# Optimization experiments

Measured on AMD Instinct MI355X. Metric: run time of the kernel, lower is better.

The kernel has to match this reference:

```python
import jax, jax.numpy as jnp
import numpy as np

B, T, D = 2, 2048, 1024
HD = 128          # head_dim
NH = 16           # num_attention_heads
NKV = 8           # num_key_value_heads
EPS = 1e-6
ROPE_THETA = 1000000.0


def setup_inputs() -> dict:
    key = jax.random.key(0)
    ks = jax.random.split(key, 7)
    s = 0.02
    return {
        "x": jax.random.normal(ks[0], (B, T, D), dtype=jnp.float32),
        "wq": jax.random.normal(ks[1], (D, NH * HD), dtype=jnp.float32) * s,
        "wk": jax.random.normal(ks[2], (D, NKV * HD), dtype=jnp.float32) * s,
        "wv": jax.random.normal(ks[3], (D, NKV * HD), dtype=jnp.float32) * s,
        "wo": jax.random.normal(ks[4], (NH * HD, D), dtype=jnp.float32) * s,
        "q_norm_w": jnp.ones((HD,), dtype=jnp.float32),
        "k_norm_w": jnp.ones((HD,), dtype=jnp.float32),
    }


def _rms_norm(x, w):
    # torch source: x / (rms + eps) * w  (eps added OUTSIDE the sqrt)
    rms = jnp.sqrt(jnp.mean(x * x, axis=-1, keepdims=True))
    return w * (x / (rms + EPS))


def _rope_cos_sin(seq_len):
    pos = jnp.arange(seq_len, dtype=jnp.float32)
    thetas = ROPE_THETA ** (-2.0 * jnp.arange(HD // 2, dtype=jnp.float32) / HD)
    freqs = pos[:, None] * thetas[None, :]            # [T, HD//2]
    return jnp.cos(freqs), jnp.sin(freqs)


def _apply_rope(x, cos, sin):
    # x: [B, H, T, HD]; interleaved complex pairs (view_as_complex layout)
    xr = x[..., 0::2]
    xi = x[..., 1::2]
    c = cos[None, None, :, :]
    s = sin[None, None, :, :]
    out_r = xr * c - xi * s
    out_i = xr * s + xi * c
    return jnp.stack([out_r, out_i], axis=-1).reshape(x.shape)


def reference(x, wq, wk, wv, wo, q_norm_w, k_norm_w):
    b, t, d = x.shape
    q = (x @ wq).reshape(b, t, NH, HD).transpose(0, 2, 1, 3)    # [B,NH,T,HD]
    k = (x @ wk).reshape(b, t, NKV, HD).transpose(0, 2, 1, 3)   # [B,NKV,T,HD]
    v = (x @ wv).reshape(b, t, NKV, HD).transpose(0, 2, 1, 3)

    q = _rms_norm(q, q_norm_w)
    k = _rms_norm(k, k_norm_w)

    rep = NH // NKV
    k = jnp.repeat(k, rep, axis=1)   # GQA expand -> [B,NH,T,HD]
    v = jnp.repeat(v, rep, axis=1)

    cos, sin = _rope_cos_sin(t)
    q = _apply_rope(q, cos, sin)
    k = _apply_rope(k, cos, sin)

    scale = 1.0 / jnp.sqrt(jnp.float32(HD))
    scores = jnp.einsum("bhqd,bhkd->bhqk", q, k) * scale        # [B,NH,T,T]
    mask = jnp.triu(jnp.full((t, t), -jnp.inf, dtype=scores.dtype), k=1)
    scores = scores + mask
    attn = jax.nn.softmax(scores.astype(jnp.float32), axis=-1).astype(q.dtype)
    y = jnp.einsum("bhqk,bhkd->bhqd", attn, v)                  # [B,NH,T,HD]
    y = y.transpose(0, 2, 1, 3).reshape(b, t, NH * HD)
    return y @ wo
```

## Files before the change

kernel.cpp:

```cpp
#include <hip/hip_runtime.h>
#include <hip/hip_bf16.h>
#include <cstdint>
#include <cstddef>

using bf16 = __hip_bfloat16;
using short8 = __attribute__((ext_vector_type(8))) short;
using f32x4  = __attribute__((ext_vector_type(4))) float;
using f32x16 = __attribute__((ext_vector_type(16))) float;

#define DEVI __device__ __forceinline__

DEVI void async_ld16(const void* g, void* l) {
  __builtin_amdgcn_global_load_lds(
      (const __attribute__((address_space(1))) unsigned int*)g,
      (__attribute__((address_space(3))) unsigned int*)l, 16, 0, 0);
}

DEVI unsigned int cvt_pk_bf16(float lo, float hi) {
  unsigned int r;
  asm("v_cvt_pk_bf16_f32 %0, %1, %2" : "=v"(r) : "v"(lo), "v"(hi));
  return r;
}

__global__ void cvt_f32_bf16(const float* __restrict__ in, bf16* __restrict__ out, int n4) {
  int i = blockIdx.x * blockDim.x + threadIdx.x;
  if (i >= n4) return;
  float4 v = ((const float4*)in)[i];
  union { bf16 h[4]; ushort4 u; } o;
  o.h[0] = __float2bfloat16(v.x);
  o.h[1] = __float2bfloat16(v.y);
  o.h[2] = __float2bfloat16(v.z);
  o.h[3] = __float2bfloat16(v.w);
  ((ushort4*)out)[i] = o.u;
}

__global__ __launch_bounds__(256) void transpose_cvt(
    const float* __restrict__ in, bf16* __restrict__ out, int K, int N) {
  __shared__ float tile[32][33];
  int n0 = blockIdx.x * 32, k0 = blockIdx.y * 32;
  int tx = threadIdx.x & 31, ty = threadIdx.x >> 5;
#pragma unroll
  for (int i = 0; i < 32; i += 8)
    tile[ty + i][tx] = in[(size_t)(k0 + ty + i) * N + n0 + tx];
  __syncthreads();
#pragma unroll
  for (int i = 0; i < 32; i += 8)
    out[(size_t)(n0 + ty + i) * K + k0 + tx] = __float2bfloat16(tile[tx][ty + i]);
}

__global__ __launch_bounds__(256) void transpose_cvt3(
    const float* __restrict__ wq, const float* __restrict__ wk,
    const float* __restrict__ wv, bf16* __restrict__ wt) {
  __shared__ float tile[32][33];
  int z = blockIdx.z;
  const float* src; int N, coff, roff;
  if (z < 2)       { src = wq; N = 2048; coff = z * 1024; roff = z * 1024; }
  else if (z == 2) { src = wk; N = 1024; coff = 0;        roff = 2048; }
  else             { src = wv; N = 1024; coff = 0;        roff = 3072; }
  int n0 = coff + blockIdx.x * 32, k0 = blockIdx.y * 32;
  int tx = threadIdx.x & 31, ty = threadIdx.x >> 5;
#pragma unroll
  for (int i = 0; i < 32; i += 8)
    tile[ty + i][tx] = src[(size_t)(k0 + ty + i) * N + n0 + tx];
  __syncthreads();
#pragma unroll
  for (int i = 0; i < 32; i += 8)
    wt[(size_t)(roff + blockIdx.x * 32 + ty + i) * 1024 + k0 + tx] =
        __float2bfloat16(tile[tx][ty + i]);
}

__global__ __launch_bounds__(256) void v_transpose(
    const bf16* __restrict__ qkv, bf16* __restrict__ Vt) {
  __shared__ bf16 tile[32][34];
  int bk = blockIdx.z;
  int t0 = blockIdx.x * 32, h0 = blockIdx.y * 32;
  int tx = threadIdx.x & 31, ty = threadIdx.x >> 5;
  int b = bk >> 3, kvh = bk & 7;
  const bf16* src = qkv + (size_t)(b * 2048) * 4096 + 3072 + kvh * 128;
#pragma unroll
  for (int i = 0; i < 32; i += 8)
    tile[ty + i][tx] = src[(size_t)(t0 + ty + i) * 4096 + h0 + tx];
  __syncthreads();
  bf16* dst = Vt + (size_t)bk * 128 * 2048;
#pragma unroll
  for (int i = 0; i < 32; i += 8)
    dst[(size_t)(h0 + ty + i) * 2048 + t0 + tx] = tile[tx][ty + i];
}

__global__ void rope_tab(float2* __restrict__ tab) {
  int t = blockIdx.x, i = threadIdx.x;
  float ex = -2.f * (float)i * (1.f / 128.f);
  float theta = exp2f(ex * 19.9315685693241741f);
  float f = (float)t * theta;
  float sv, cv;
  sincosf(f, &sv, &cv);
  tab[t * 64 + i] = make_float2(cv, sv);
}

__global__ __launch_bounds__(256, 4) void gemm_bt4(
    const bf16* __restrict__ A, const bf16* __restrict__ Bt,
    bf16* __restrict__ C, int M, int N, int K) {
  __shared__ alignas(16) bf16 As[128 * 64];
  __shared__ alignas(16) bf16 Bs[128 * 64];
  const int tid = threadIdx.x, lane = tid & 63, w = tid >> 6;
  const int wm = w >> 1, wn = w & 1;
  const int m0 = blockIdx.y * 128, n0 = blockIdx.x * 128;
  const int nt = K >> 6;
  f32x4 acc[4][4] = {};

  const int srow = lane >> 3;
  const int scb  = (lane & 7) * 16;

  for (int kt = 0; kt < nt; ++kt) {
#pragma unroll
    for (int i = 0; i < 4; i++) {
      int row = w * 32 + i * 8 + srow;
      int src_cb = scb ^ ((row & 7) << 4);
      async_ld16((const char*)(A  + (size_t)(m0 + row) * K + kt * 64) + src_cb,
                 (char*)As + w * 4096 + i * 1024);
      async_ld16((const char*)(Bt + (size_t)(n0 + row) * K + kt * 64) + src_cb,
                 (char*)Bs + w * 4096 + i * 1024);
    }
    asm volatile("s_waitcnt vmcnt(0)" ::: "memory");
    __builtin_amdgcn_s_barrier();
#pragma unroll
    for (int ks = 0; ks < 2; ks++) {
      short8 af[4], bfr[4];
#pragma unroll
      for (int mi = 0; mi < 4; mi++) {
        int row = wm * 64 + mi * 16 + (lane & 15);
        int cb = (ks * 64 + (lane >> 4) * 16) ^ ((row & 7) << 4);
        af[mi] = *(const short8*)((const char*)As + row * 128 + cb);
      }
#pragma unroll
      for (int ni = 0; ni < 4; ni++) {
        int row = wn * 64 + ni * 16 + (lane & 15);
        int cb = (ks * 64 + (lane >> 4) * 16) ^ ((row & 7) << 4);
        bfr[ni] = *(const short8*)((const char*)Bs + row * 128 + cb);
      }
#pragma unroll
      for (int mi = 0; mi < 4; mi++)
#pragma unroll
        for (int ni = 0; ni < 4; ni++)
          acc[mi][ni] = __builtin_amdgcn_mfma_f32_16x16x32_bf16(af[mi], bfr[ni], acc[mi][ni], 0, 0, 0);
    }
    __builtin_amdgcn_s_barrier();
    __builtin_amdgcn_sched_barrier(0);
  }

  const int c0 = n0 + wn * 64 + (lane & 15);
  const int r0 = m0 + wm * 64 + (lane >> 4) * 4;
#pragma unroll
  for (int mi = 0; mi < 4; mi++)
#pragma unroll
    for (int ni = 0; ni < 4; ni++)
#pragma unroll
      for (int r = 0; r < 4; r++) {
        size_t idx = (size_t)(r0 + mi * 16 + r) * N + (c0 + ni * 16);
        C[idx] = __float2bfloat16(acc[mi][ni][r]);
      }
}

__global__ __launch_bounds__(256, 2) void gemm_out(
    const bf16* __restrict__ A, const bf16* __restrict__ Bt,
    float* __restrict__ C, int M, int N, int K) {
  __shared__ alignas(16) bf16 As[2][128 * 64];
  __shared__ alignas(16) bf16 Bs[2][128 * 64];
  const int tid = threadIdx.x, lane = tid & 63, w = tid >> 6;
  const int wm = w >> 1, wn = w & 1;
  const int m0 = blockIdx.y * 128, n0 = blockIdx.x * 128;
  const int nt = K >> 6;
  f32x4 acc[4][4] = {};

  const int srow = lane >> 3;
  const int scb  = (lane & 7) * 16;

  auto stage = [&](int buf, int kt) {
#pragma unroll
    for (int i = 0; i < 4; i++) {
      int row = w * 32 + i * 8 + srow;
      int src_cb = scb ^ ((row & 7) << 4);
      async_ld16((const char*)(A  + (size_t)(m0 + row) * K + kt * 64) + src_cb,
                 (char*)As[buf] + w * 4096 + i * 1024);
      async_ld16((const char*)(Bt + (size_t)(n0 + row) * K + kt * 64) + src_cb,
                 (char*)Bs[buf] + w * 4096 + i * 1024);
    }
  };

  stage(0, 0);
  stage(1, 1);

  for (int kt = 0; kt < nt; ++kt) {
    const int buf = kt & 1;
    if (kt + 1 < nt) asm volatile("s_waitcnt vmcnt(8)" ::: "memory");
    else             asm volatile("s_waitcnt vmcnt(0)" ::: "memory");
    __builtin_amdgcn_s_barrier();
#pragma unroll
    for (int ks = 0; ks < 2; ks++) {
      short8 af[4], bfr[4];
#pragma unroll
      for (int mi = 0; mi < 4; mi++) {
        int row = wm * 64 + mi * 16 + (lane & 15);
        int cb = (ks * 64 + (lane >> 4) * 16) ^ ((row & 7) << 4);
        af[mi] = *(const short8*)((const char*)As[buf] + row * 128 + cb);
      }
#pragma unroll
      for (int ni = 0; ni < 4; ni++) {
        int row = wn * 64 + ni * 16 + (lane & 15);
        int cb = (ks * 64 + (lane >> 4) * 16) ^ ((row & 7) << 4);
        bfr[ni] = *(const short8*)((const char*)Bs[buf] + row * 128 + cb);
      }
#pragma unroll
      for (int mi = 0; mi < 4; mi++)
#pragma unroll
        for (int ni = 0; ni < 4; ni++)
          acc[mi][ni] = __builtin_amdgcn_mfma_f32_16x16x32_bf16(af[mi], bfr[ni], acc[mi][ni], 0, 0, 0);
    }
    __builtin_amdgcn_s_barrier();
    __builtin_amdgcn_sched_barrier(0);
    if (kt + 2 < nt) stage(buf, kt + 2);
  }

  const int c0 = n0 + wn * 64 + (lane & 15);
  const int r0 = m0 + wm * 64 + (lane >> 4) * 4;
#pragma unroll
  for (int mi = 0; mi < 4; mi++)
#pragma unroll
    for (int ni = 0; ni < 4; ni++)
#pragma unroll
      for (int r = 0; r < 4; r++)
        C[(size_t)(r0 + mi * 16 + r) * N + (c0 + ni * 16)] = acc[mi][ni][r];
}

__global__ __launch_bounds__(256) void norm_rope(
    const bf16* __restrict__ qkv, const float* __restrict__ qw, const float* __restrict__ kw,
    const float2* __restrict__ tab,
    bf16* __restrict__ Qh, bf16* __restrict__ Kh) {
  const int w = threadIdx.x >> 6, lane = threadIdx.x & 63;
  const int grp = lane >> 4, l = lane & 15;
  const int flat = blockIdx.x * 16 + w * 4 + grp;
  const int m = flat / 24, slot = flat - m * 24;
  const int b = m >> 11, t = m & 2047;

  const int type = slot >= 16;
  const int h = type ? slot - 16 : slot;
  const int col = type ? 2048 + h * 128 : h * 128;

  union { short8 s; bf16 h[8]; } u;
  u.s = *(const short8*)(qkv + (size_t)m * 4096 + col + l * 8);
  float x[8];
#pragma unroll
  for (int j = 0; j < 8; j++) x[j] = __bfloat162float(u.h[j]);

  float ss = 0.f;
#pragma unroll
  for (int j = 0; j < 8; j++) ss += x[j] * x[j];
#pragma unroll
  for (int o = 1; o < 16; o <<= 1) ss += __shfl_xor(ss, o);
  float rms = sqrtf(ss * (1.f / 128.f));
  float inv = 1.f / (rms + 1e-6f);
  if (!type) inv *= 0.12751744416163417f;

  const float* wn = type ? kw : qw;
  float4 w0 = *(const float4*)(wn + l * 8);
  float4 w1 = *(const float4*)(wn + l * 8 + 4);
  float wv[8] = {w0.x, w0.y, w0.z, w0.w, w1.x, w1.y, w1.z, w1.w};

  const float4* tb = (const float4*)(tab + t * 64 + l * 4);
  float4 t0 = tb[0], t1 = tb[1];
  float cs[8] = {t0.x, t0.y, t0.z, t0.w, t1.x, t1.y, t1.z, t1.w};

  union { short8 s; bf16 h[8]; } o;
#pragma unroll
  for (int i = 0; i < 4; i++) {
    float re = wv[2 * i] * x[2 * i] * inv;
    float im = wv[2 * i + 1] * x[2 * i + 1] * inv;
    float c = cs[2 * i], s = cs[2 * i + 1];
    o.h[2 * i]     = __float2bfloat16(re * c - im * s);
    o.h[2 * i + 1] = __float2bfloat16(re * s + im * c);
  }
  bf16* dst = type
      ? Kh + ((size_t)(b * 8 + h) * 2048 + t) * 128 + l * 8
      : Qh + ((size_t)(b * 16 + h) * 2048 + t) * 128 + l * 8;
  *(short8*)dst = o.s;
}

__global__ __launch_bounds__(512, 1) void flash_attn10(
    const bf16* __restrict__ Qh, const bf16* __restrict__ Kh,
    const bf16* __restrict__ Vt, bf16* __restrict__ Y) {
  __shared__ alignas(16) bf16 KB[4][64 * 128];
  __shared__ alignas(16) bf16 VB[4][128 * 64];
  __shared__ float MLs[128][2];
  const int tid = threadIdx.x, lane = tid & 63, w = tid >> 6;
  const int hi = lane >> 5, lq = lane & 31;
  const int grp = w >> 2, wl = w & 3;

  const int g = blockIdx.x;
  const int bh = (g & 7) * 4 + ((g >> 3) & 3);
  const int p  = g >> 5;
  const int b = bh >> 4, h = bh & 15, kvh = h >> 1;

  const bf16* Qg = Qh + (size_t)(b * 16 + h) * 2048 * 128;
  const bf16* Kg = Kh + (size_t)(b * 8 + kvh) * 2048 * 128;
  const bf16* Vg = Vt + (size_t)(b * 8 + kvh) * 128 * 2048;

  short8 qf[8];
  f32x16 oacc[4];
  float m, l;
  int qw = 0, qg = 0;

  auto stage2 = [&](int set, int k0e) {
#pragma unroll
    for (int gb = 0; gb < 2; gb++) {
      const int k0 = k0e + gb * 64;
      char* kb = (char*)KB[set * 2 + gb];
      char* vb = (char*)VB[set * 2 + gb];
#pragma unroll
      for (int i = 0; i < 2; i++) {
        int c = w * 2 + i;
        {
          int row = c * 4 + (lane >> 4);
          int cb = ((lane & 15) * 16) ^ ((row & 7) << 4);
          async_ld16((const char*)Kg + (size_t)(k0 + row) * 256 + cb, kb + c * 1024);
        }
        {
          int row = c * 8 + (lane >> 3);
          int cb = ((lane & 7) * 16) ^ ((row & 7) << 4);
          async_ld16((const char*)Vg + (size_t)row * 4096 + (size_t)k0 * 2 + cb, vb + c * 1024);
        }
      }
    }
  };

  auto setupTile = [&](int q0) {
    qw = q0 + wl * 32;
    qg = qw + lq;
#pragma unroll
    for (int dc = 0; dc < 8; dc++)
      qf[dc] = *(const short8*)(Qg + (size_t)qg * 128 + dc * 16 + hi * 8);
#pragma unroll
    for (int dc = 0; dc < 4; dc++)
#pragma unroll
      for (int r = 0; r < 16; r++) oacc[dc][r] = 0.f;
    m = -1e30f;
    l = 0.f;
  };

  auto computeStep = [&](int bufI, int k0) {
    f32x16 st[2] = {};
#pragma unroll
    for (int kc = 0; kc < 2; kc++) {
      int row = kc * 32 + lq;
      int swz = (row & 7) << 4;
      const char* kbase = (const char*)KB[bufI] + row * 256;
#pragma unroll
      for (int dc = 0; dc < 8; dc++) {
        short8 kf = *(const short8*)(kbase + ((dc * 32 + hi * 16) ^ swz));
        st[kc] = __builtin_amdgcn_mfma_f32_32x32x16_bf16(kf, qf[dc], st[kc], 0, 0, 0);
      }
    }
    const bool msk = (k0 + 63 > qw);
    if (msk) {
#pragma unroll
      for (int kc = 0; kc < 2; kc++)
#pragma unroll
        for (int rr = 0; rr < 16; rr++) {
          int kg = k0 + kc * 32 + (rr & 3) + 8 * (rr >> 2) + 4 * hi;
          if (kg > qg) st[kc][rr] = -1e30f;
        }
    }
    float mx[16];
#pragma unroll
    for (int rr = 0; rr < 16; rr++) mx[rr] = fmaxf(st[0][rr], st[1][rr]);
#pragma unroll
    for (int off = 8; off >= 1; off >>= 1)
#pragma unroll
      for (int rr = 0; rr < 8; rr++)
        if (rr < off) mx[rr] = fmaxf(mx[rr], mx[rr + off]);
    float pm = fmaxf(mx[0], __shfl_xor(mx[0], 32));
    if (__any(pm > m + 8.f)) {
      float mnew = fmaxf(m, pm);
      float alpha = exp2f(m - mnew);
      m = mnew;
      l *= alpha;
      float al[16];
#pragma unroll
      for (int rr = 0; rr < 16; rr++)
        al[rr] = __shfl(alpha, (rr & 3) + 8 * (rr >> 2) + 4 * hi);
#pragma unroll
      for (int dc = 0; dc < 4; dc++)
#pragma unroll
        for (int rr = 0; rr < 16; rr++) oacc[dc][rr] *= al[rr];
    }
#pragma unroll
    for (int kc = 0; kc < 2; kc++)
#pragma unroll
      for (int rr = 0; rr < 16; rr++) st[kc][rr] = exp2f(st[kc][rr] - m);
    float sm[16];
#pragma unroll
    for (int rr = 0; rr < 16; rr++) sm[rr] = st[0][rr] + st[1][rr];
#pragma unroll
    for (int off = 8; off >= 1; off >>= 1)
#pragma unroll
      for (int rr = 0; rr < 8; rr++)
        if (rr < off) sm[rr] += sm[rr + off];
    l += sm[0] + __shfl_xor(sm[0], 32);
    short8 af[4];
#pragma unroll
    for (int kc = 0; kc < 2; kc++)
#pragma unroll
      for (int sb = 0; sb < 2; sb++) {
        int base = sb * 8;
        unsigned int a01 = cvt_pk_bf16(st[kc][base + 0], st[kc][base + 1]);
        unsigned int a23 = cvt_pk_bf16(st[kc][base + 2], st[kc][base + 3]);
        unsigned int b01 = cvt_pk_bf16(st[kc][base + 4], st[kc][base + 5]);
        unsigned int b23 = cvt_pk_bf16(st[kc][base + 6], st[kc][base + 7]);
        unsigned int xa01 = (unsigned int)__shfl_xor((int)a01, 32);
        unsigned int xa23 = (unsigned int)__shfl_xor((int)a23, 32);
        unsigned int xb01 = (unsigned int)__shfl_xor((int)b01, 32);
        unsigned int xb23 = (unsigned int)__shfl_xor((int)b23, 32);
        union { unsigned int u[4]; short8 s; } f;
        f.u[0] = hi ? xb01 : a01;
        f.u[1] = hi ? xb23 : a23;
        f.u[2] = hi ? b01 : xa01;
        f.u[3] = hi ? b23 : xa23;
        af[kc * 2 + sb] = f.s;
      }
#pragma unroll
    for (int dc = 0; dc < 4; dc++) {
      int row = dc * 32 + lq;
      int swz = (row & 7) << 4;
      const char* vbase = (const char*)VB[bufI] + row * 128;
#pragma unroll
      for (int ks = 0; ks < 4; ks++) {
        short8 vf = *(const short8*)(vbase + ((ks * 32 + hi * 16) ^ swz));
        oacc[dc] = __builtin_amdgcn_mfma_f32_32x32x16_bf16(af[ks], vf, oacc[dc], 0, 0, 0);
      }
    }
  };

  auto runRounds = [&](int n) {
    const int R = n >> 1;
    for (int r = 0; r < R; ++r) {
      asm volatile("s_waitcnt vmcnt(0)" ::: "memory");
      __builtin_amdgcn_s_barrier();
      if (r + 1 < R) stage2((r + 1) & 1, (2 * r + 2) * 64);
      __builtin_amdgcn_sched_barrier(0);
      const int s = 2 * r + grp, k0 = s * 64;
      const int bufI = (r & 1) * 2 + grp;
      if (k0 < qw + 32) computeStep(bufI, k0);
    }
  };

  auto writePartials = [&]() {
    float* base = (wl < 2) ? (float*)KB[2] : (float*)VB[2];
#pragma unroll
    for (int dc = 0; dc < 4; dc++)
#pragma unroll
      for (int rr = 0; rr < 16; rr++) {
        int q = (wl & 1) * 32 + (rr & 3) + 8 * (rr >> 2) + 4 * hi;
        base[q * 128 + dc * 32 + lq] = oacc[dc][rr];
      }
    if (lane < 32) {
      MLs[wl * 32 + lane][0] = m;
      MLs[wl * 32 + lane][1] = l;
    }
  };

  auto mergeAndY = [&](int q0) {
    float m1 = MLs[wl * 32 + lq][0], l1 = MLs[wl * 32 + lq][1];
    float mN = fmaxf(m, m1);
    float e0 = exp2f(m - mN), e1 = exp2f(m1 - mN);
    float lT = l * e0 + l1 * e1;
    float inv = 1.f / lT;
    float e0r[16], e1r[16], ivr[16];
#pragma unroll
    for (int rr = 0; rr < 16; rr++) {
      int src = (rr & 3) + 8 * (rr >> 2) + 4 * hi;
      e0r[rr] = __shfl(e0, src);
      e1r[rr] = __shfl(e1, src);
      ivr[rr] = __shfl(inv, src);
    }
    const float* base = (wl < 2) ? (const float*)KB[2] : (const float*)VB[2];
#pragma unroll
    for (int dc = 0; dc < 4; dc++)
#pragma unroll
      for (int rr = 0; rr < 16; rr++) {
        int q = (wl & 1) * 32 + (rr & 3) + 8 * (rr >> 2) + 4 * hi;
        float o1 = base[q * 128 + dc * 32 + lq];
        float oT = oacc[dc][rr] * e0r[rr] + o1 * e1r[rr];
        int t = q0 + wl * 32 + (rr & 3) + 8 * (rr >> 2) + 4 * hi;
        Y[(size_t)(b * 2048 + t) * 2048 + h * 128 + dc * 32 + lq] =
            __float2bfloat16(oT * ivr[rr]);
      }
  };

  const int jA = 15 - p, jB = p;
  const int q0A = jA * 128, nA = 2 * jA + 2;
  const int q0B = jB * 128, nB = 2 * jB + 2;

  setupTile(q0A);
  stage2(0, 0);
  runRounds(nA);
  __syncthreads();
  stage2(0, 0);
  if (grp == 1) writePartials();
  __syncthreads();
  if (grp == 0) mergeAndY(q0A);
  setupTile(q0B);
  runRounds(nB);
  __syncthreads();
  if (grp == 1) writePartials();
  __syncthreads();
  if (grp == 0) mergeAndY(q0B);
}

extern "C" void kernel_launch(void* const* d_in, const int* in_sizes, int n_in,
                              void* d_out, int out_size, void* d_ws, size_t ws_size,
                              hipStream_t stream) {
  (void)in_sizes; (void)n_in; (void)out_size; (void)ws_size;
  const float* x   = (const float*)d_in[0];
  const float* wq  = (const float*)d_in[1];
  const float* wk  = (const float*)d_in[2];
  const float* wv  = (const float*)d_in[3];
  const float* wo  = (const float*)d_in[4];
  const float* qnw = (const float*)d_in[5];
  const float* knw = (const float*)d_in[6];
  float* out = (float*)d_out;
  char* ws = (char*)d_ws;
  const size_t MB = 1u << 20;
  bf16*   xb  = (bf16*)(ws + 0 * MB);
  bf16*   wt  = (bf16*)(ws + 8 * MB);
  bf16*   wot = (bf16*)(ws + 16 * MB);
  bf16*   qkv = (bf16*)(ws + 20 * MB);
  float2* tab = (float2*)(ws + 52 * MB);
  bf16*   Qh  = (bf16*)(ws + 53 * MB);
  bf16*   Kh  = (bf16*)(ws + 69 * MB);
  bf16*   Vtr = (bf16*)(ws + 77 * MB);
  bf16*   Yb  = (bf16*)(ws + 85 * MB);

  cvt_f32_bf16<<<4096, 256, 0, stream>>>(x, xb, 1048576);
  transpose_cvt3<<<dim3(32, 32, 4), 256, 0, stream>>>(wq, wk, wv, wt);
  transpose_cvt<<<dim3(32, 64), 256, 0, stream>>>(wo, wot, 2048, 1024);
  rope_tab<<<2048, 64, 0, stream>>>(tab);
  gemm_bt4<<<dim3(32, 32), 256, 0, stream>>>(xb, wt, qkv, 4096, 4096, 1024);
  norm_rope<<<6144, 256, 0, stream>>>(qkv, qnw, knw, tab, Qh, Kh);
  v_transpose<<<dim3(64, 4, 16), 256, 0, stream>>>(qkv, Vtr);
  flash_attn10<<<256, 512, 0, stream>>>(Qh, Kh, Vtr, Yb);
  gemm_out<<<dim3(8, 32), 256, 0, stream>>>(Yb, wot, out, 4096, 1024, 2048);
}
```

Measured before the change: 176.8 us.

## Fuse QK norm, RoPE and V transpose into double-buffered QKV GEMM epilogue

```diff
diff --git a/kernel.cpp b/kernel.cpp
--- a/kernel.cpp
+++ b/kernel.cpp
@@ -69,24 +69,6 @@
         __float2bfloat16(tile[tx][ty + i]);
 }
 
-__global__ __launch_bounds__(256) void v_transpose(
-    const bf16* __restrict__ qkv, bf16* __restrict__ Vt) {
-  __shared__ bf16 tile[32][34];
-  int bk = blockIdx.z;
-  int t0 = blockIdx.x * 32, h0 = blockIdx.y * 32;
-  int tx = threadIdx.x & 31, ty = threadIdx.x >> 5;
-  int b = bk >> 3, kvh = bk & 7;
-  const bf16* src = qkv + (size_t)(b * 2048) * 4096 + 3072 + kvh * 128;
-#pragma unroll
-  for (int i = 0; i < 32; i += 8)
-    tile[ty + i][tx] = src[(size_t)(t0 + ty + i) * 4096 + h0 + tx];
-  __syncthreads();
-  bf16* dst = Vt + (size_t)bk * 128 * 2048;
-#pragma unroll
-  for (int i = 0; i < 32; i += 8)
-    dst[(size_t)(h0 + ty + i) * 2048 + t0 + tx] = tile[tx][ty + i];
-}
-
 __global__ void rope_tab(float2* __restrict__ tab) {
   int t = blockIdx.x, i = threadIdx.x;
   float ex = -2.f * (float)i * (1.f / 128.f);
@@ -97,31 +79,42 @@
   tab[t * 64 + i] = make_float2(cv, sv);
 }
 
-__global__ __launch_bounds__(256, 4) void gemm_bt4(
+__global__ __launch_bounds__(256, 2) void gemm_qkv(
     const bf16* __restrict__ A, const bf16* __restrict__ Bt,
-    bf16* __restrict__ C, int M, int N, int K) {
-  __shared__ alignas(16) bf16 As[128 * 64];
-  __shared__ alignas(16) bf16 Bs[128 * 64];
+    const float* __restrict__ qnw, const float* __restrict__ knw,
+    const float2* __restrict__ tab,
+    bf16* __restrict__ Qh, bf16* __restrict__ Kh, bf16* __restrict__ Vt) {
+  __shared__ alignas(16) bf16 As[2][128 * 64];
+  __shared__ alignas(16) bf16 Bs[2][128 * 64];
   const int tid = threadIdx.x, lane = tid & 63, w = tid >> 6;
   const int wm = w >> 1, wn = w & 1;
-  const int m0 = blockIdx.y * 128, n0 = blockIdx.x * 128;
-  const int nt = K >> 6;
+  const int bx = blockIdx.x;
+  const int m0 = blockIdx.y * 128, n0 = bx * 128;
+  const int K = 1024, nt = 16;
   f32x4 acc[4][4] = {};
 
   const int srow = lane >> 3;
   const int scb  = (lane & 7) * 16;
 
-  for (int kt = 0; kt < nt; ++kt) {
+  auto stage = [&](int buf, int kt) {
 #pragma unroll
     for (int i = 0; i < 4; i++) {
       int row = w * 32 + i * 8 + srow;
       int src_cb = scb ^ ((row & 7) << 4);
       async_ld16((const char*)(A  + (size_t)(m0 + row) * K + kt * 64) + src_cb,
-                 (char*)As + w * 4096 + i * 1024);
+                 (char*)As[buf] + w * 4096 + i * 1024);
       async_ld16((const char*)(Bt + (size_t)(n0 + row) * K + kt * 64) + src_cb,
-                 (char*)Bs + w * 4096 + i * 1024);
-    }
-    asm volatile("s_waitcnt vmcnt(0)" ::: "memory");
+                 (char*)Bs[buf] + w * 4096 + i * 1024);
+    }
+  };
+
+  stage(0, 0);
+  stage(1, 1);
+
+  for (int kt = 0; kt < nt; ++kt) {
+    const int buf = kt & 1;
+    if (kt + 1 < nt) asm volatile("s_waitcnt vmcnt(8)" ::: "memory");
+    else             asm volatile("s_waitcnt vmcnt(0)" ::: "memory");
     __builtin_amdgcn_s_barrier();
 #pragma unroll
     for (int ks = 0; ks < 2; ks++) {
@@ -130,13 +123,13 @@
       for (int mi = 0; mi < 4; mi++) {
         int row = wm * 64 + mi * 16 + (lane & 15);
         int cb = (ks * 64 + (lane >> 4) * 16) ^ ((row & 7) << 4);
-        af[mi] = *(const short8*)((const char*)As + row * 128 + cb);
+        af[mi] = *(const short8*)((const char*)As[buf] + row * 128 + cb);
       }
 #pragma unroll
       for (int ni = 0; ni < 4; ni++) {
         int row = wn * 64 + ni * 16 + (lane & 15);
         int cb = (ks * 64 + (lane >> 4) * 16) ^ ((row & 7) << 4);
-        bfr[ni] = *(const short8*)((const char*)Bs + row * 128 + cb);
+        bfr[ni] = *(const short8*)((const char*)Bs[buf] + row * 128 + cb);
       }
 #pragma unroll
       for (int mi = 0; mi < 4; mi++)
@@ -146,19 +139,92 @@
     }
     __builtin_amdgcn_s_barrier();
     __builtin_amdgcn_sched_barrier(0);
+    if (kt + 2 < nt) stage(buf, kt + 2);
   }
 
-  const int c0 = n0 + wn * 64 + (lane & 15);
-  const int r0 = m0 + wm * 64 + (lane >> 4) * 4;
-#pragma unroll
-  for (int mi = 0; mi < 4; mi++)
-#pragma unroll
-    for (int ni = 0; ni < 4; ni++)
+  const int b = m0 >> 11;
+
+  if (bx < 24) {
+    __syncthreads();
+    float* ssb = (float*)As;
+    float s[4][4];
+#pragma unroll
+    for (int mi = 0; mi < 4; mi++)
 #pragma unroll
       for (int r = 0; r < 4; r++) {
-        size_t idx = (size_t)(r0 + mi * 16 + r) * N + (c0 + ni * 16);
-        C[idx] = __float2bfloat16(acc[mi][ni][r]);
-      }
+        float v0 = acc[mi][0][r], v1 = acc[mi][1][r];
+        float v2 = acc[mi][2][r], v3 = acc[mi][3][r];
+        float t = v0 * v0 + v1 * v1 + v2 * v2 + v3 * v3;
+        t += __shfl_xor(t, 1);
+        t += __shfl_xor(t, 2);
+        t += __shfl_xor(t, 4);
+        t += __shfl_xor(t, 8);
+        s[mi][r] = t;
+      }
+    if ((lane & 15) == 0) {
+#pragma unroll
+      for (int mi = 0; mi < 4; mi++)
+#pragma unroll
+        for (int r = 0; r < 4; r++)
+          ssb[wn * 128 + wm * 64 + mi * 16 + (lane >> 4) * 4 + r] = s[mi][r];
+    }
+    __syncthreads();
+
+    const int isQ = (bx < 16);
+    const int h = isQ ? bx : bx - 16;
+    const float* wnp = isQ ? qnw : knw;
+    bf16* dst = isQ ? Qh : Kh;
+    const int NHH = isQ ? 16 : 8;
+    const float qs = isQ ? 0.12751744416163417f : 1.f;
+    float wd[4];
+#pragma unroll
+    for (int ni = 0; ni < 4; ni++) wd[ni] = wnp[wn * 64 + ni * 16 + (lane & 15)];
+
+#pragma unroll
+    for (int mi = 0; mi < 4; mi++)
+#pragma unroll
+      for (int r = 0; r < 4; r++) {
+        int rl = wm * 64 + mi * 16 + (lane >> 4) * 4 + r;
+        float tot = ssb[rl] + ssb[128 + rl];
+        float inv = qs / (sqrtf(tot * 0.0078125f) + 1e-6f);
+        int t = (m0 + rl) & 2047;
+        bf16* drow = dst + ((size_t)(b * NHH + h) * 2048 + t) * 128;
+#pragma unroll
+        for (int ni = 0; ni < 4; ni++) {
+          int d = wn * 64 + ni * 16 + (lane & 15);
+          float val = acc[mi][ni][r] * inv * wd[ni];
+          float prt = __shfl_xor(val, 1);
+          float2 cs = tab[t * 64 + (d >> 1)];
+          float o = (d & 1) ? (prt * cs.y + val * cs.x)
+                            : (val * cs.x - prt * cs.y);
+          drow[d] = __float2bfloat16(o);
+        }
+      }
+  } else {
+    __syncthreads();
+    bf16* vt = (bf16*)As;
+    const int vh = bx - 24;
+#pragma unroll
+    for (int mi = 0; mi < 4; mi++)
+#pragma unroll
+      for (int ni = 0; ni < 4; ni++) {
+        int d = wn * 64 + ni * 16 + (lane & 15);
+        int tl = wm * 64 + mi * 16 + (lane >> 4) * 4;
+        unsigned int p0 = cvt_pk_bf16(acc[mi][ni][0], acc[mi][ni][1]);
+        unsigned int p1 = cvt_pk_bf16(acc[mi][ni][2], acc[mi][ni][3]);
+        int byte = d * 256 + ((tl * 2) ^ ((d & 7) << 4));
+        *(uint2*)((char*)vt + byte) = make_uint2(p0, p1);
+      }
+    __syncthreads();
+    bf16* dstV = Vt + (size_t)(b * 8 + vh) * 128 * 2048 + (m0 & 2047);
+#pragma unroll
+    for (int i = 0; i < 8; i++) {
+      int flat = tid + i * 256;
+      int d = flat >> 4, g = flat & 15;
+      short8 v = *(const short8*)((const char*)vt + d * 256 + ((g * 16) ^ ((d & 7) << 4)));
+      *(short8*)(dstV + (size_t)d * 2048 + g * 8) = v;
+    }
+  }
 }
 
 __global__ __launch_bounds__(256, 2) void gemm_out(
@@ -230,59 +296,6 @@
 #pragma unroll
       for (int r = 0; r < 4; r++)
         C[(size_t)(r0 + mi * 16 + r) * N + (c0 + ni * 16)] = acc[mi][ni][r];
-}
-
-__global__ __launch_bounds__(256) void norm_rope(
-    const bf16* __restrict__ qkv, const float* __restrict__ qw, const float* __restrict__ kw,
-    const float2* __restrict__ tab,
-    bf16* __restrict__ Qh, bf16* __restrict__ Kh) {
-  const int w = threadIdx.x >> 6, lane = threadIdx.x & 63;
-  const int grp = lane >> 4, l = lane & 15;
-  const int flat = blockIdx.x * 16 + w * 4 + grp;
-  const int m = flat / 24, slot = flat - m * 24;
-  const int b = m >> 11, t = m & 2047;
-
-  const int type = slot >= 16;
-  const int h = type ? slot - 16 : slot;
-  const int col = type ? 2048 + h * 128 : h * 128;
-
-  union { short8 s; bf16 h[8]; } u;
-  u.s = *(const short8*)(qkv + (size_t)m * 4096 + col + l * 8);
-  float x[8];
-#pragma unroll
-  for (int j = 0; j < 8; j++) x[j] = __bfloat162float(u.h[j]);
-
-  float ss = 0.f;
-#pragma unroll
-  for (int j = 0; j < 8; j++) ss += x[j] * x[j];
-#pragma unroll
-  for (int o = 1; o < 16; o <<= 1) ss += __shfl_xor(ss, o);
-  float rms = sqrtf(ss * (1.f / 128.f));
-  float inv = 1.f / (rms + 1e-6f);
-  if (!type) inv *= 0.12751744416163417f;
-
-  const float* wn = type ? kw : qw;
-  float4 w0 = *(const float4*)(wn + l * 8);
-  float4 w1 = *(const float4*)(wn + l * 8 + 4);
-  float wv[8] = {w0.x, w0.y, w0.z, w0.w, w1.x, w1.y, w1.z, w1.w};
-
-  const float4* tb = (const float4*)(tab + t * 64 + l * 4);
-  float4 t0 = tb[0], t1 = tb[1];
-  float cs[8] = {t0.x, t0.y, t0.z, t0.w, t1.x, t1.y, t1.z, t1.w};
-
-  union { short8 s; bf16 h[8]; } o;
-#pragma unroll
-  for (int i = 0; i < 4; i++) {
-    float re = wv[2 * i] * x[2 * i] * inv;
-    float im = wv[2 * i + 1] * x[2 * i + 1] * inv;
-    float c = cs[2 * i], s = cs[2 * i + 1];
-    o.h[2 * i]     = __float2bfloat16(re * c - im * s);
-    o.h[2 * i + 1] = __float2bfloat16(re * s + im * c);
-  }
-  bf16* dst = type
-      ? Kh + ((size_t)(b * 8 + h) * 2048 + t) * 128 + l * 8
-      : Qh + ((size_t)(b * 16 + h) * 2048 + t) * 128 + l * 8;
-  *(short8*)dst = o.s;
 }
 
 __global__ __launch_bounds__(512, 1) void flash_attn10(
@@ -532,7 +545,6 @@
   bf16*   xb  = (bf16*)(ws + 0 * MB);
   bf16*   wt  = (bf16*)(ws + 8 * MB);
   bf16*   wot = (bf16*)(ws + 16 * MB);
-  bf16*   qkv = (bf16*)(ws + 20 * MB);
   float2* tab = (float2*)(ws + 52 * MB);
   bf16*   Qh  = (bf16*)(ws + 53 * MB);
   bf16*   Kh  = (bf16*)(ws + 69 * MB);
@@ -543,9 +555,7 @@
   transpose_cvt3<<<dim3(32, 32, 4), 256, 0, stream>>>(wq, wk, wv, wt);
   transpose_cvt<<<dim3(32, 64), 256, 0, stream>>>(wo, wot, 2048, 1024);
   rope_tab<<<2048, 64, 0, stream>>>(tab);
-  gemm_bt4<<<dim3(32, 32), 256, 0, stream>>>(xb, wt, qkv, 4096, 4096, 1024);
-  norm_rope<<<6144, 256, 0, stream>>>(qkv, qnw, knw, tab, Qh, Kh);
-  v_transpose<<<dim3(64, 4, 16), 256, 0, stream>>>(qkv, Vtr);
+  gemm_qkv<<<dim3(32, 32), 256, 0, stream>>>(xb, wt, qnw, knw, tab, Qh, Kh, Vtr);
   flash_attn10<<<256, 512, 0, stream>>>(Qh, Kh, Vtr, Yb);
   gemm_out<<<dim3(8, 32), 256, 0, stream>>>(Yb, wot, out, 4096, 1024, 2048);
 }
```

Measured after the change: 166.6 us. 5.8% less time.
